# Optimization experiments

Hardware: AMD Instinct MI355X
Metric: run time of the kernel (lower is better)

Reference implementation:

```python
import jax, jax.numpy as jnp
import numpy as np

G, A, HID, NF, L = 512, 32, 256, 11, 4
EMB = HID - 1  # embed_dim = in_node_nf - 1 (condition_time)


def _forward(node_feat, pos, t,
             enc_w1, enc_b1, enc_w2, enc_b2,
             ew1, eb1, ew2, eb2,
             xw1, xb1, xw2, xb2,
             hw1, hb1, hw2, hb2,
             rg1, rgb1, rv1, rvb1, rg2, rgb2, rv2, rvb2, rw3, rb3,
             batch, edge_src, edge_dst):
    silu = jax.nn.silu
    N = node_feat.shape[0]
    # remove_mean_batch: subtract per-graph centroid (scatter_mean)
    cnt = jax.ops.segment_sum(jnp.ones((N, 1), pos.dtype), batch, num_segments=G)
    mean = jax.ops.segment_sum(pos, batch, num_segments=G) / cnt
    x0 = pos - mean[batch]
    # fragment encoder MLP (last layer no activation): 11 -> 22 -> 255
    h = silu(node_feat @ enc_w1 + enc_b1) @ enc_w2 + enc_b2
    # condition on time (t scalar broadcast to all nodes)
    h = jnp.concatenate([h, jnp.full((N, 1), t[0], h.dtype)], axis=1)  # [N, 256]
    x = x0
    for l in range(L):  # EGNN message-passing layers
        hi, hj = h[edge_src], h[edge_dst]
        rel = x[edge_src] - x[edge_dst]                    # [E, 3]
        d2 = jnp.sum(rel * rel, axis=-1, keepdims=True)    # [E, 1]
        e_in = jnp.concatenate([hi, hj, d2], axis=1)       # [E, 2*HID+1]
        m = silu(silu(e_in @ ew1[l] + eb1[l]) @ ew2[l] + eb2[l])  # edge MLP phi_e
        agg = jax.ops.segment_sum(m, edge_src, num_segments=N)
        coef = silu(m @ xw1[l] + xb1[l]) @ xw2[l] + xb2[l]        # phi_x -> [E,1]
        # subgraph_mask is all ones (single fragment), coord update equivariant
        x = x + jax.ops.segment_sum(rel * coef, edge_src, num_segments=N)
        h = h + silu(jnp.concatenate([h, agg], axis=1) @ hw1[l] + hb1[l]) @ hw2[l] + hb2[l]
    # GatedMLP readout: 256 -> 256 -> 256 -> 1, last layer plain linear
    g = silu(h @ rg1 + rgb1) * (h @ rv1 + rvb1)
    g = silu(g @ rg2 + rgb2) * (g @ rv2 + rvb2)
    y = g @ rw3 + rb3                                      # [N, 1]
    ae = jax.ops.segment_sum(y, batch, num_segments=G)[:, 0]  # per-graph energy
    forces = x - x0                                        # equivariant coord displacement
    return ae, forces


def setup_inputs() -> dict:
    key = jax.random.key(0)
    kc = [0]
    def nk():
        kc[0] += 1
        return jax.random.fold_in(key, kc[0])
    N = G * A
    node_feat = jax.random.normal(nk(), (N, NF), jnp.float32)
    pos = jax.random.normal(nk(), (N, 3), jnp.float32) * 3.0
    batch = jnp.repeat(jnp.arange(G), A)
    # fully-connected intra-graph edges without self loops (get_edges_index)
    i = np.arange(A)
    s, d = np.meshgrid(i, i, indexing='ij')
    msk = s != d
    s, d = s[msk], d[msk]
    offs = (np.arange(G) * A)[:, None]
    edge_src = jnp.asarray((s[None, :] + offs).reshape(-1))
    edge_dst = jnp.asarray((d[None, :] + offs).reshape(-1))
    def lin(fi, fo):
        return jax.random.normal(nk(), (fi, fo), jnp.float32) / np.sqrt(fi)
    def linL(fi, fo):
        return jax.random.normal(nk(), (L, fi, fo), jnp.float32) / np.sqrt(fi)
    inp = dict(node_feat=node_feat, pos=pos, t=jnp.zeros((1,), jnp.float32),
               enc_w1=lin(NF, 2 * NF), enc_b1=jnp.zeros((2 * NF,), jnp.float32),
               enc_w2=lin(2 * NF, EMB), enc_b2=jnp.zeros((EMB,), jnp.float32),
               ew1=linL(2 * HID + 1, HID), eb1=jnp.zeros((L, HID), jnp.float32),
               ew2=linL(HID, HID), eb2=jnp.zeros((L, HID), jnp.float32),
               xw1=linL(HID, HID), xb1=jnp.zeros((L, HID), jnp.float32),
               xw2=linL(HID, 1) * 0.1, xb2=jnp.zeros((L, 1), jnp.float32),
               hw1=linL(2 * HID, HID), hb1=jnp.zeros((L, HID), jnp.float32),
               hw2=linL(HID, HID), hb2=jnp.zeros((L, HID), jnp.float32),
               rg1=lin(HID, HID), rgb1=jnp.zeros((HID,), jnp.float32),
               rv1=lin(HID, HID), rvb1=jnp.zeros((HID,), jnp.float32),
               rg2=lin(HID, HID), rgb2=jnp.zeros((HID,), jnp.float32),
               rv2=lin(HID, HID), rvb2=jnp.zeros((HID,), jnp.float32),
               rw3=lin(HID, 1), rb3=jnp.zeros((1,), jnp.float32),
               batch=batch, edge_src=edge_src, edge_dst=edge_dst)
    return inp


def reference(node_feat, pos, t,
              enc_w1, enc_b1, enc_w2, enc_b2,
              ew1, eb1, ew2, eb2,
              xw1, xb1, xw2, xb2,
              hw1, hb1, hw2, hb2,
              rg1, rgb1, rv1, rvb1, rg2, rgb2, rv2, rvb2, rw3, rb3,
              batch, edge_src, edge_dst):
    return _forward(node_feat, pos, t,
                    enc_w1, enc_b1, enc_w2, enc_b2,
                    ew1, eb1, ew2, eb2,
                    xw1, xb1, xw2, xb2,
                    hw1, hb1, hw2, hb2,
                    rg1, rgb1, rv1, rvb1, rg2, rgb2, rv2, rvb2, rw3, rb3,
                    batch, edge_src, edge_dst)
```

## Files before the change

### kernel.cpp

```cpp
#include <hip/hip_runtime.h>

#define NGRAPH 512
#define NA 32
#define HID 256
#define NT 512
#define NLAYER 4

using short8 = __attribute__((ext_vector_type(8))) short;
using f32x4  = __attribute__((ext_vector_type(4))) float;

#define MFMA(a,b,c) __builtin_amdgcn_mfma_f32_16x16x32_bf16((a),(b),(c),0,0,0)

__device__ __forceinline__ float CL(float x) {
    return fminf(fmaxf(x, -1e15f), 1e15f);
}
__device__ __forceinline__ float silu_f(float x) {
    return x / (1.0f + __expf(-x));
}
__device__ __forceinline__ unsigned short bf16t(float x) {
    return (unsigned short)(__float_as_uint(x) >> 16);
}
__device__ __forceinline__ float up16(unsigned short u) {
    return __uint_as_float(((unsigned)u) << 16);
}

__device__ __forceinline__ short8 ldA(const unsigned short* sA, int row, int kk, int sg) {
    return *(const short8*)(sA + row*256 + ((kk*32 + sg*8) ^ ((row & 7) << 3)));
}

__device__ __forceinline__ short8 ldBfrag(const float* __restrict__ W,
                                          int kk, int nt, int li, int sg) {
    const float* p = W + (size_t)(kk*32 + sg*8)*HID + nt*16 + li;
    short8 r;
#pragma unroll
    for (int e = 0; e < 8; ++e) r[e] = (short)bf16t(p[(size_t)e*HID]);
    return r;
}

extern "C" __global__ void __launch_bounds__(NT, 2)
egnn_mfma(const float* __restrict__ node_feat, const float* __restrict__ pos,
          const float* __restrict__ tt,
          const float* __restrict__ enc_w1, const float* __restrict__ enc_b1,
          const float* __restrict__ enc_w2, const float* __restrict__ enc_b2,
          const float* __restrict__ ew1, const float* __restrict__ eb1,
          const float* __restrict__ ew2, const float* __restrict__ eb2,
          const float* __restrict__ xw1, const float* __restrict__ xb1,
          const float* __restrict__ xw2, const float* __restrict__ xb2,
          const float* __restrict__ hw1, const float* __restrict__ hb1,
          const float* __restrict__ hw2, const float* __restrict__ hb2,
          const float* __restrict__ rg1, const float* __restrict__ rgb1,
          const float* __restrict__ rv1, const float* __restrict__ rvb1,
          const float* __restrict__ rg2, const float* __restrict__ rgb2,
          const float* __restrict__ rv2, const float* __restrict__ rvb2,
          const float* __restrict__ rw3, const float* __restrict__ rb3,
          float* __restrict__ out)
{
    __shared__ float          sH  [NA*HID];
    __shared__ unsigned short sPa [NA*HID];
    __shared__ unsigned short sPb [NA*HID];
    __shared__ unsigned short sAgg[NA*HID];
    __shared__ unsigned short sAb [64*HID];
    __shared__ float sW1d[HID];
    __shared__ float sB1 [HID];
    __shared__ float sh_x[NA*3], sh_x0[NA*3], sh_dx[NA*3];
    __shared__ float sh_d2[64], sh_coef[64];
    __shared__ float sh_a1[NA*22];
    __shared__ float sh_red[8];

    const int g    = blockIdx.x;
    const int tid  = threadIdx.x;
    const int w    = tid >> 6;
    const int lane = tid & 63;
    const int li   = lane & 15;
    const int sg   = lane >> 4;
    const int nb   = g * NA;

    if (tid < NA) {
        float px = pos[(nb+tid)*3+0], py = pos[(nb+tid)*3+1], pz = pos[(nb+tid)*3+2];
        float sx = px, sy = py, sz = pz;
#pragma unroll
        for (int m = 1; m < 32; m <<= 1) {
            sx += __shfl_xor(sx, m); sy += __shfl_xor(sy, m); sz += __shfl_xor(sz, m);
        }
        const float inv = 1.0f/32.0f;
        const float xx = px - sx*inv, xy = py - sy*inv, xz = pz - sz*inv;
        sh_x [tid*3+0]=xx; sh_x [tid*3+1]=xy; sh_x [tid*3+2]=xz;
        sh_x0[tid*3+0]=xx; sh_x0[tid*3+1]=xy; sh_x0[tid*3+2]=xz;
        sh_dx[tid*3+0]=0.f; sh_dx[tid*3+1]=0.f; sh_dx[tid*3+2]=0.f;
    }

    for (int e = tid; e < NA*22; e += NT) {
        const int node = e / 22, u = e - node*22;
        const float* nfp = node_feat + (size_t)(nb+node)*11;
        float s = enc_b1[u];
#pragma unroll
        for (int f = 0; f < 11; ++f) s = fmaf(nfp[f], enc_w1[f*22+u], s);
        sh_a1[e] = CL(silu_f(s));
    }
    __syncthreads();
    for (int e = tid; e < NA*255; e += NT) {
        const int node = e / 255, o = e - node*255;
        const float* ap = sh_a1 + node*22;
        float s = enc_b2[o];
#pragma unroll
        for (int u = 0; u < 22; ++u) s = fmaf(ap[u], enc_w2[u*255+o], s);
        sH[node*HID + o] = CL(s);
    }
    if (tid < NA) sH[tid*HID + 255] = tt[0];
    __syncthreads();

    for (int l = 0; l < NLAYER; ++l) {
        const float* W1   = ew1 + (size_t)l*513*HID;
        const float* W1b  = W1 + 256*HID;
        const float* b1v  = eb1 + l*HID;
        const float* W2   = ew2 + (size_t)l*HID*HID;
        const float* b2v  = eb2 + l*HID;
        const float* XW1  = xw1 + (size_t)l*HID*HID;
        const float* xb1v = xb1 + l*HID;
        const float* XW2  = xw2 + (size_t)l*HID;
        const float  xb2v = xb2[l];
        const float* HW1a = hw1 + (size_t)l*2*HID*HID;
        const float* HW1b = HW1a + 256*HID;
        const float* hb1v = hb1 + l*HID;
        const float* HW2  = hw2 + (size_t)l*HID*HID;
        const float* hb2v = hb2 + l*HID;

        for (int t2 = tid; t2 < 1024; t2 += NT) {
            const int row = t2 >> 5, c = t2 & 31;
            const float* hp = sH + row*HID + c*8;
            short8 o;
#pragma unroll
            for (int e = 0; e < 8; ++e) o[e] = (short)bf16t(hp[e]);
            *(short8*)(sAb + row*256 + ((c*8) ^ ((row & 7) << 3))) = o;
        }
        if (tid < HID) { sW1d[tid] = W1[512*HID + tid]; sB1[tid] = b1v[tid]; }
        __syncthreads();

        {
            const int mg = w >> 2, ng = w & 3;
            f32x4 aA[4] = {}, aB[4] = {};
#pragma unroll
            for (int kk = 0; kk < 8; ++kk) {
                short8 a = ldA(sAb, mg*16 + li, kk, sg);
#pragma unroll
                for (int q = 0; q < 4; ++q) {
                    aA[q] = MFMA(a, ldBfrag(W1,  kk, ng*4+q, li, sg), aA[q]);
                    aB[q] = MFMA(a, ldBfrag(W1b, kk, ng*4+q, li, sg), aB[q]);
                }
            }
#pragma unroll
            for (int q = 0; q < 4; ++q) {
                const int col = (ng*4+q)*16 + li;
#pragma unroll
                for (int r = 0; r < 4; ++r) {
                    const int row = mg*16 + sg*4 + r;
                    sPa[row*256 + col] = bf16t(CL(aA[q][r]));
                    sPb[row*256 + col] = bf16t(CL(aB[q][r]));
                }
            }
        }
        short8 w2f[16], x1f[16];
#pragma unroll
        for (int kk = 0; kk < 8; ++kk)
#pragma unroll
            for (int q = 0; q < 2; ++q) {
                w2f[kk*2+q] = ldBfrag(W2,  kk, w*2+q, li, sg);
                x1f[kk*2+q] = ldBfrag(XW1, kk, w*2+q, li, sg);
            }
        __syncthreads();

        for (int pair = 0; pair < 16; ++pair) {
            const int i0 = pair*2;
            if (tid < 64) {
                const int ip = tid >> 5, j = tid & 31, ig = i0 + ip;
                const float rx = sh_x[ig*3+0]-sh_x[j*3+0];
                const float ry = sh_x[ig*3+1]-sh_x[j*3+1];
                const float rz = sh_x[ig*3+2]-sh_x[j*3+2];
                sh_d2[tid] = rx*rx + ry*ry + rz*rz;
                sh_coef[tid] = 0.f;
            }
            __syncthreads();

            {
                const int c = tid & 31, rg = tid >> 5;
                const float4* wp = (const float4*)(sW1d + c*8);
                const float4* bp = (const float4*)(sB1 + c*8);
                const float4 w0 = wp[0], w1 = wp[1], b0 = bp[0], b1 = bp[1];
                float wd[8] = {w0.x,w0.y,w0.z,w0.w,w1.x,w1.y,w1.z,w1.w};
                float bb[8] = {b0.x,b0.y,b0.z,b0.w,b1.x,b1.y,b1.z,b1.w};
#pragma unroll
                for (int k = 0; k < 4; ++k) {
                    const int row = rg + 16*k;
                    const int ip = row >> 5, j = row & 31;
                    const short8 pa8 = *(const short8*)(sPa + (i0+ip)*256 + c*8);
                    const short8 pb8 = *(const short8*)(sPb + j*256 + c*8);
                    const float d2v = sh_d2[row];
                    short8 o;
#pragma unroll
                    for (int e = 0; e < 8; ++e) {
                        float x = up16((unsigned short)pa8[e]) + up16((unsigned short)pb8[e])
                                + d2v*wd[e] + bb[e];
                        o[e] = (short)bf16t(CL(silu_f(x)));
                    }
                    *(short8*)(sAb + row*256 + ((c*8) ^ ((row & 7) << 3))) = o;
                }
            }
            __syncthreads();

            f32x4 a1[4][2] = {};
#pragma unroll
            for (int kk = 0; kk < 8; ++kk)
#pragma unroll
                for (int mt = 0; mt < 4; ++mt) {
                    short8 a = ldA(sAb, mt*16 + li, kk, sg);
                    a1[mt][0] = MFMA(a, w2f[kk*2+0], a1[mt][0]);
                    a1[mt][1] = MFMA(a, w2f[kk*2+1], a1[mt][1]);
                }
#pragma unroll
            for (int q = 0; q < 2; ++q) {
                const float b2c = b2v[(w*2+q)*16 + li];
#pragma unroll
                for (int mt = 0; mt < 4; ++mt)
#pragma unroll
                    for (int r = 0; r < 4; ++r)
                        a1[mt][q][r] = CL(silu_f(a1[mt][q][r] + b2c));
            }
#pragma unroll
            for (int ip = 0; ip < 2; ++ip) {
                const int ig = i0 + ip;
                const int drow = ip*32 + ig;
#pragma unroll
                for (int q = 0; q < 2; ++q) {
                    float s = 0.f;
#pragma unroll
                    for (int mt2 = 0; mt2 < 2; ++mt2) {
                        const int mt = ip*2 + mt2;
#pragma unroll
                        for (int r = 0; r < 4; ++r) {
                            const int row = mt*16 + sg*4 + r;
                            s += (row == drow) ? 0.f : a1[mt][q][r];
                        }
                    }
                    s += __shfl_xor(s, 16);
                    s += __shfl_xor(s, 32);
                    if (lane < 16) {
                        const int col = (w*2+q)*16 + lane;
                        sAgg[ig*256 + (col ^ ((ig & 7) << 3))] = bf16t(CL(s));
                    }
                }
            }
            __syncthreads();

#pragma unroll
            for (int q = 0; q < 2; ++q) {
                const int col = (w*2+q)*16 + li;
#pragma unroll
                for (int mt = 0; mt < 4; ++mt)
#pragma unroll
                    for (int r = 0; r < 4; ++r) {
                        const int row = mt*16 + sg*4 + r;
                        sAb[row*256 + (col ^ ((row & 7) << 3))] = bf16t(a1[mt][q][r]);
                    }
            }
            __syncthreads();

            f32x4 a2[4][2] = {};
#pragma unroll
            for (int kk = 0; kk < 8; ++kk)
#pragma unroll
                for (int mt = 0; mt < 4; ++mt) {
                    short8 a = ldA(sAb, mt*16 + li, kk, sg);
                    a2[mt][0] = MFMA(a, x1f[kk*2+0], a2[mt][0]);
                    a2[mt][1] = MFMA(a, x1f[kk*2+1], a2[mt][1]);
                }
            {
                const float xbc0 = xb1v[(w*2+0)*16 + li], xwc0 = XW2[(w*2+0)*16 + li];
                const float xbc1 = xb1v[(w*2+1)*16 + li], xwc1 = XW2[(w*2+1)*16 + li];
#pragma unroll
                for (int mt = 0; mt < 4; ++mt) {
                    float p[4];
#pragma unroll
                    for (int r = 0; r < 4; ++r)
                        p[r] = silu_f(a2[mt][0][r] + xbc0) * xwc0
                             + silu_f(a2[mt][1][r] + xbc1) * xwc1;
#pragma unroll
                    for (int r = 0; r < 4; ++r) {
                        float v = p[r];
                        v += __shfl_xor(v, 1); v += __shfl_xor(v, 2);
                        v += __shfl_xor(v, 4); v += __shfl_xor(v, 8);
                        if (li == 0) atomicAdd(&sh_coef[mt*16 + sg*4 + r], CL(v));
                    }
                }
            }
            __syncthreads();

            if (tid < 64) {
                const int ip = tid >> 5, j = tid & 31, ig = i0 + ip;
                const float cf = CL(sh_coef[tid] + xb2v);
                const float rx = sh_x[ig*3+0]-sh_x[j*3+0];
                const float ry = sh_x[ig*3+1]-sh_x[j*3+1];
                const float rz = sh_x[ig*3+2]-sh_x[j*3+2];
                const bool diag = (j == ig);
                float vx = diag ? 0.f : rx*cf;
                float vy = diag ? 0.f : ry*cf;
                float vz = diag ? 0.f : rz*cf;
#pragma unroll
                for (int m = 1; m < 32; m <<= 1) {
                    vx += __shfl_xor(vx, m); vy += __shfl_xor(vy, m); vz += __shfl_xor(vz, m);
                }
                if ((tid & 31) == 0) {
                    sh_dx[ig*3+0] = CL(sh_dx[ig*3+0] + vx);
                    sh_dx[ig*3+1] = CL(sh_dx[ig*3+1] + vy);
                    sh_dx[ig*3+2] = CL(sh_dx[ig*3+2] + vz);
                }
            }
            __syncthreads();
        }

        for (int t2 = tid; t2 < 1024; t2 += NT) {
            const int row = t2 >> 5, c = t2 & 31;
            const float* hp = sH + row*HID + c*8;
            short8 o;
#pragma unroll
            for (int e = 0; e < 8; ++e) o[e] = (short)bf16t(hp[e]);
            *(short8*)(sAb + row*256 + ((c*8) ^ ((row & 7) << 3))) = o;
        }
        if (tid < NA*3) { sh_x[tid] = CL(sh_x[tid] + sh_dx[tid]); sh_dx[tid] = 0.f; }
        __syncthreads();

        {
            const int mg = w >> 2, ng = w & 3;
            f32x4 u[4] = {};
#pragma unroll
            for (int kk = 0; kk < 8; ++kk) {
                short8 ah = ldA(sAb,  mg*16 + li, kk, sg);
                short8 ag = ldA(sAgg, mg*16 + li, kk, sg);
#pragma unroll
                for (int q = 0; q < 4; ++q) {
                    u[q] = MFMA(ah, ldBfrag(HW1a, kk, ng*4+q, li, sg), u[q]);
                    u[q] = MFMA(ag, ldBfrag(HW1b, kk, ng*4+q, li, sg), u[q]);
                }
            }
#pragma unroll
            for (int q = 0; q < 4; ++q) {
                const int col = (ng*4+q)*16 + li;
                const float bc = hb1v[col];
#pragma unroll
                for (int r = 0; r < 4; ++r) {
                    const int row32 = 32 + mg*16 + sg*4 + r;
                    sAb[row32*256 + (col ^ ((row32 & 7) << 3))] =
                        bf16t(CL(silu_f(u[q][r] + bc)));
                }
            }
            __syncthreads();
            f32x4 d[4] = {};
#pragma unroll
            for (int kk = 0; kk < 8; ++kk) {
                short8 a = ldA(sAb, 32 + mg*16 + li, kk, sg);
#pragma unroll
                for (int q = 0; q < 4; ++q)
                    d[q] = MFMA(a, ldBfrag(HW2, kk, ng*4+q, li, sg), d[q]);
            }
#pragma unroll
            for (int q = 0; q < 4; ++q) {
                const int col = (ng*4+q)*16 + li;
                const float bc = hb2v[col];
#pragma unroll
                for (int r = 0; r < 4; ++r) {
                    const int idx = (mg*16 + sg*4 + r)*HID + col;
                    sH[idx] = CL(sH[idx] + d[q][r] + bc);
                }
            }
        }
        __syncthreads();
    }

    for (int t2 = tid; t2 < 1024; t2 += NT) {
        const int row = t2 >> 5, c = t2 & 31;
        const float* hp = sH + row*HID + c*8;
        short8 o;
#pragma unroll
        for (int e = 0; e < 8; ++e) o[e] = (short)bf16t(hp[e]);
        *(short8*)(sAb + row*256 + ((c*8) ^ ((row & 7) << 3))) = o;
    }
    __syncthreads();
    {
        const int mg = w >> 2, ng = w & 3;
        f32x4 ga[4] = {}, gb[4] = {};
#pragma unroll
        for (int kk = 0; kk < 8; ++kk) {
            short8 a = ldA(sAb, mg*16 + li, kk, sg);
#pragma unroll
            for (int q = 0; q < 4; ++q) {
                ga[q] = MFMA(a, ldBfrag(rg1, kk, ng*4+q, li, sg), ga[q]);
                gb[q] = MFMA(a, ldBfrag(rv1, kk, ng*4+q, li, sg), gb[q]);
            }
        }
#pragma unroll
        for (int q = 0; q < 4; ++q) {
            const int col = (ng*4+q)*16 + li;
            const float bg = rgb1[col], bv = rvb1[col];
#pragma unroll
            for (int r = 0; r < 4; ++r) {
                const int row32 = 32 + mg*16 + sg*4 + r;
                sAb[row32*256 + (col ^ ((row32 & 7) << 3))] =
                    bf16t(CL(silu_f(ga[q][r] + bg) * (gb[q][r] + bv)));
            }
        }
        __syncthreads();
        f32x4 g2a[4] = {}, g2b[4] = {};
#pragma unroll
        for (int kk = 0; kk < 8; ++kk) {
            short8 a = ldA(sAb, 32 + mg*16 + li, kk, sg);
#pragma unroll
            for (int q = 0; q < 4; ++q) {
                g2a[q] = MFMA(a, ldBfrag(rg2, kk, ng*4+q, li, sg), g2a[q]);
                g2b[q] = MFMA(a, ldBfrag(rv2, kk, ng*4+q, li, sg), g2b[q]);
            }
        }
        float p = 0.f;
#pragma unroll
        for (int q = 0; q < 4; ++q) {
            const int col = (ng*4+q)*16 + li;
            const float bg = rgb2[col], bv = rvb2[col], rw = rw3[col];
#pragma unroll
            for (int r = 0; r < 4; ++r)
                p += CL(silu_f(g2a[q][r] + bg) * (g2b[q][r] + bv)) * rw;
        }
        p = CL(p);
#pragma unroll
        for (int m = 1; m < 64; m <<= 1) p += __shfl_xor(p, m);
        if (lane == 0) sh_red[w] = p;
        __syncthreads();
        if (tid == 0) {
            float s = 0.f;
#pragma unroll
            for (int ww = 0; ww < 8; ++ww) s += sh_red[ww];
            out[g] = s + (float)NA * rb3[0];
        }
    }
    if (tid < NA*3) out[NGRAPH + g*(NA*3) + tid] = sh_x[tid] - sh_x0[tid];
}

extern "C" __global__ void egnn_node_pad1() {}
extern "C" __global__ void egnn_node_pad2() {}

extern "C" void kernel_launch(void* const* d_in, const int* in_sizes, int n_in,
                              void* d_out, int out_size, void* d_ws, size_t ws_size,
                              hipStream_t stream)
{
    const float* node_feat = (const float*)d_in[0];
    const float* pos    = (const float*)d_in[1];
    const float* tt     = (const float*)d_in[2];
    const float* enc_w1 = (const float*)d_in[3];
    const float* enc_b1 = (const float*)d_in[4];
    const float* enc_w2 = (const float*)d_in[5];
    const float* enc_b2 = (const float*)d_in[6];
    const float* ew1    = (const float*)d_in[7];
    const float* eb1    = (const float*)d_in[8];
    const float* ew2    = (const float*)d_in[9];
    const float* eb2    = (const float*)d_in[10];
    const float* xw1    = (const float*)d_in[11];
    const float* xb1    = (const float*)d_in[12];
    const float* xw2    = (const float*)d_in[13];
    const float* xb2    = (const float*)d_in[14];
    const float* hw1    = (const float*)d_in[15];
    const float* hb1    = (const float*)d_in[16];
    const float* hw2    = (const float*)d_in[17];
    const float* hb2    = (const float*)d_in[18];
    const float* rg1    = (const float*)d_in[19];
    const float* rgb1   = (const float*)d_in[20];
    const float* rv1    = (const float*)d_in[21];
    const float* rvb1   = (const float*)d_in[22];
    const float* rg2    = (const float*)d_in[23];
    const float* rgb2   = (const float*)d_in[24];
    const float* rv2    = (const float*)d_in[25];
    const float* rvb2   = (const float*)d_in[26];
    const float* rw3    = (const float*)d_in[27];
    const float* rb3    = (const float*)d_in[28];
    (void)d_ws; (void)ws_size; (void)in_sizes; (void)n_in;

    egnn_mfma<<<NGRAPH, NT, 0, stream>>>(
        node_feat, pos, tt, enc_w1, enc_b1, enc_w2, enc_b2,
        ew1, eb1, ew2, eb2, xw1, xb1, xw2, xb2,
        hw1, hb1, hw2, hb2, rg1, rgb1, rv1, rvb1,
        rg2, rgb2, rv2, rvb2, rw3, rb3,
        (float*)d_out);
    egnn_node_pad1<<<1, 64, 0, stream>>>();
    egnn_node_pad2<<<1, 64, 0, stream>>>();
}
```

Measured before the change: 2.454 ms.

## Store node features as bf16, split GEMMs by weight half, precompute pairwise distances

Node hidden state is now kept in shared memory as swizzled bf16 instead of fp32, which removes the per-layer fp32-to-bf16 conversion passes. The node-level GEMMs are redistributed so each wave group handles one weight half (or gate/value matrix) over all 32 rows. Each B fragment is therefore loaded once and reused across two row tiles, and partial sums are combined through an fp32 scratch buffer aliased onto sAb. Pairwise squared distances are computed once per layer, and the coefficient buffer is double-buffered, which drops one barrier per pair iteration. Rounding the residual stream to bf16 adds precision loss, and the extra reduction barriers plus the shared-memory layout changes could affect occupancy.

```diff
diff --git a/kernel.cpp b/kernel.cpp
--- a/kernel.cpp
+++ b/kernel.cpp
@@ -23,11 +23,12 @@
 __device__ __forceinline__ float up16(unsigned short u) {
     return __uint_as_float(((unsigned)u) << 16);
 }
-
+__device__ __forceinline__ int swzi(int row, int col) {
+    return row*256 + (col ^ ((row & 7) << 3));
+}
 __device__ __forceinline__ short8 ldA(const unsigned short* sA, int row, int kk, int sg) {
     return *(const short8*)(sA + row*256 + ((kk*32 + sg*8) ^ ((row & 7) << 3)));
 }
-
 __device__ __forceinline__ short8 ldBfrag(const float* __restrict__ W,
                                           int kk, int nt, int li, int sg) {
     const float* p = W + (size_t)(kk*32 + sg*8)*HID + nt*16 + li;
@@ -37,7 +38,8 @@
     return r;
 }
 
-extern "C" __global__ void __launch_bounds__(NT, 2)
+extern "C" __global__ void __launch_bounds__(NT)
+__attribute__((amdgpu_waves_per_eu(2, 2)))
 egnn_mfma(const float* __restrict__ node_feat, const float* __restrict__ pos,
           const float* __restrict__ tt,
           const float* __restrict__ enc_w1, const float* __restrict__ enc_b1,
@@ -55,17 +57,19 @@
           const float* __restrict__ rw3, const float* __restrict__ rb3,
           float* __restrict__ out)
 {
-    __shared__ float          sH  [NA*HID];
+    __shared__ unsigned short sHb [NA*HID];
     __shared__ unsigned short sPa [NA*HID];
     __shared__ unsigned short sPb [NA*HID];
     __shared__ unsigned short sAgg[NA*HID];
-    __shared__ unsigned short sAb [64*HID];
-    __shared__ float sW1d[HID];
-    __shared__ float sB1 [HID];
+    __shared__ unsigned short sAb [2*NA*HID];
+    __shared__ float sD2[NA*NA];
+    __shared__ float sW1d[HID], sB1[HID];
     __shared__ float sh_x[NA*3], sh_x0[NA*3], sh_dx[NA*3];
-    __shared__ float sh_d2[64], sh_coef[64];
+    __shared__ float sh_coef[2][64];
     __shared__ float sh_a1[NA*22];
     __shared__ float sh_red[8];
+
+    float* sF = (float*)sAb;
 
     const int g    = blockIdx.x;
     const int tid  = threadIdx.x;
@@ -79,8 +83,8 @@
         float px = pos[(nb+tid)*3+0], py = pos[(nb+tid)*3+1], pz = pos[(nb+tid)*3+2];
         float sx = px, sy = py, sz = pz;
 #pragma unroll
-        for (int m = 1; m < 32; m <<= 1) {
-            sx += __shfl_xor(sx, m); sy += __shfl_xor(sy, m); sz += __shfl_xor(sz, m);
+        for (int mm = 1; mm < 32; mm <<= 1) {
+            sx += __shfl_xor(sx, mm); sy += __shfl_xor(sy, mm); sz += __shfl_xor(sz, mm);
         }
         const float inv = 1.0f/32.0f;
         const float xx = px - sx*inv, xy = py - sy*inv, xz = pz - sz*inv;
@@ -104,14 +108,13 @@
         float s = enc_b2[o];
 #pragma unroll
         for (int u = 0; u < 22; ++u) s = fmaf(ap[u], enc_w2[u*255+o], s);
-        sH[node*HID + o] = CL(s);
+        sHb[swzi(node, o)] = bf16t(CL(s));
     }
-    if (tid < NA) sH[tid*HID + 255] = tt[0];
+    if (tid < NA) sHb[swzi(tid, 255)] = bf16t(tt[0]);
     __syncthreads();
 
     for (int l = 0; l < NLAYER; ++l) {
         const float* W1   = ew1 + (size_t)l*513*HID;
-        const float* W1b  = W1 + 256*HID;
         const float* b1v  = eb1 + l*HID;
         const float* W2   = ew2 + (size_t)l*HID*HID;
         const float* b2v  = eb2 + l*HID;
@@ -119,45 +122,46 @@
         const float* xb1v = xb1 + l*HID;
         const float* XW2  = xw2 + (size_t)l*HID;
         const float  xb2v = xb2[l];
-        const float* HW1a = hw1 + (size_t)l*2*HID*HID;
-        const float* HW1b = HW1a + 256*HID;
+        const float* HW1  = hw1 + (size_t)l*2*HID*HID;
         const float* hb1v = hb1 + l*HID;
         const float* HW2  = hw2 + (size_t)l*HID*HID;
         const float* hb2v = hb2 + l*HID;
 
-        for (int t2 = tid; t2 < 1024; t2 += NT) {
-            const int row = t2 >> 5, c = t2 & 31;
-            const float* hp = sH + row*HID + c*8;
-            short8 o;
-#pragma unroll
-            for (int e = 0; e < 8; ++e) o[e] = (short)bf16t(hp[e]);
-            *(short8*)(sAb + row*256 + ((c*8) ^ ((row & 7) << 3))) = o;
+        for (int e = tid; e < NA*NA; e += NT) {
+            const int i = e >> 5, j = e & 31;
+            const float rx = sh_x[i*3+0]-sh_x[j*3+0];
+            const float ry = sh_x[i*3+1]-sh_x[j*3+1];
+            const float rz = sh_x[i*3+2]-sh_x[j*3+2];
+            sD2[e] = rx*rx + ry*ry + rz*rz;
         }
         if (tid < HID) { sW1d[tid] = W1[512*HID + tid]; sB1[tid] = b1v[tid]; }
-        __syncthreads();
 
         {
-            const int mg = w >> 2, ng = w & 3;
-            f32x4 aA[4] = {}, aB[4] = {};
+            const int m = w >> 2, s = w & 3;
+            const float* Wm = W1 + (size_t)m*256*HID;
+            f32x4 acc[2][4] = {};
 #pragma unroll
             for (int kk = 0; kk < 8; ++kk) {
-                short8 a = ldA(sAb, mg*16 + li, kk, sg);
+                const short8 a0 = ldA(sHb, li,      kk, sg);
+                const short8 a1_= ldA(sHb, 16 + li, kk, sg);
 #pragma unroll
                 for (int q = 0; q < 4; ++q) {
-                    aA[q] = MFMA(a, ldBfrag(W1,  kk, ng*4+q, li, sg), aA[q]);
-                    aB[q] = MFMA(a, ldBfrag(W1b, kk, ng*4+q, li, sg), aB[q]);
-                }
-            }
-#pragma unroll
-            for (int q = 0; q < 4; ++q) {
-                const int col = (ng*4+q)*16 + li;
-#pragma unroll
-                for (int r = 0; r < 4; ++r) {
-                    const int row = mg*16 + sg*4 + r;
-                    sPa[row*256 + col] = bf16t(CL(aA[q][r]));
-                    sPb[row*256 + col] = bf16t(CL(aB[q][r]));
-                }
-            }
+                    const short8 b = ldBfrag(Wm, kk, s*4+q, li, sg);
+                    acc[0][q] = MFMA(a0,  b, acc[0][q]);
+                    acc[1][q] = MFMA(a1_, b, acc[1][q]);
+                }
+            }
+            unsigned short* dst = m ? sPb : sPa;
+#pragma unroll
+            for (int mt = 0; mt < 2; ++mt)
+#pragma unroll
+                for (int q = 0; q < 4; ++q)
+#pragma unroll
+                    for (int r = 0; r < 4; ++r) {
+                        const int row = mt*16 + sg*4 + r;
+                        const int col = (s*4+q)*16 + li;
+                        dst[swzi(row, col)] = bf16t(CL(acc[mt][q][r]));
+                    }
         }
         short8 w2f[16], x1f[16];
 #pragma unroll
@@ -167,42 +171,43 @@
                 w2f[kk*2+q] = ldBfrag(W2,  kk, w*2+q, li, sg);
                 x1f[kk*2+q] = ldBfrag(XW1, kk, w*2+q, li, sg);
             }
+        const float b2c[2] = { b2v[(w*2+0)*16+li],  b2v[(w*2+1)*16+li]  };
+        const float xbc[2] = { xb1v[(w*2+0)*16+li], xb1v[(w*2+1)*16+li] };
+        const float xwc[2] = { XW2[(w*2+0)*16+li],  XW2[(w*2+1)*16+li]  };
         __syncthreads();
 
-        for (int pair = 0; pair < 16; ++pair) {
+        int par = 0;
+        for (int pair = 0; pair < 16; ++pair, par ^= 1) {
             const int i0 = pair*2;
-            if (tid < 64) {
-                const int ip = tid >> 5, j = tid & 31, ig = i0 + ip;
-                const float rx = sh_x[ig*3+0]-sh_x[j*3+0];
-                const float ry = sh_x[ig*3+1]-sh_x[j*3+1];
-                const float rz = sh_x[ig*3+2]-sh_x[j*3+2];
-                sh_d2[tid] = rx*rx + ry*ry + rz*rz;
-                sh_coef[tid] = 0.f;
-            }
-            __syncthreads();
-
+            if (tid < 64) sh_coef[par][tid] = 0.f;
             {
                 const int c = tid & 31, rg = tid >> 5;
                 const float4* wp = (const float4*)(sW1d + c*8);
                 const float4* bp = (const float4*)(sB1 + c*8);
-                const float4 w0 = wp[0], w1 = wp[1], b0 = bp[0], b1 = bp[1];
-                float wd[8] = {w0.x,w0.y,w0.z,w0.w,w1.x,w1.y,w1.z,w1.w};
-                float bb[8] = {b0.x,b0.y,b0.z,b0.w,b1.x,b1.y,b1.z,b1.w};
+                const float4 w0 = wp[0], w1 = wp[1], bq0 = bp[0], bq1 = bp[1];
+                const float wd[8] = {w0.x,w0.y,w0.z,w0.w,w1.x,w1.y,w1.z,w1.w};
+                const float bb[8] = {bq0.x,bq0.y,bq0.z,bq0.w,bq1.x,bq1.y,bq1.z,bq1.w};
+                const short8 paA = *(const short8*)(sPa + (i0+0)*256 + ((c*8) ^ (((i0+0)&7)<<3)));
+                const short8 paB = *(const short8*)(sPa + (i0+1)*256 + ((c*8) ^ (((i0+1)&7)<<3)));
+                float pab0[8], pab1[8];
+#pragma unroll
+                for (int e = 0; e < 8; ++e) {
+                    pab0[e] = up16((unsigned short)paA[e]) + bb[e];
+                    pab1[e] = up16((unsigned short)paB[e]) + bb[e];
+                }
 #pragma unroll
                 for (int k = 0; k < 4; ++k) {
                     const int row = rg + 16*k;
-                    const int ip = row >> 5, j = row & 31;
-                    const short8 pa8 = *(const short8*)(sPa + (i0+ip)*256 + c*8);
-                    const short8 pb8 = *(const short8*)(sPb + j*256 + c*8);
-                    const float d2v = sh_d2[row];
+                    const int j   = rg + 16*(k & 1);
+                    const float d2v = sD2[(i0 + (k>>1))*32 + j];
+                    const short8 pb8 = *(const short8*)(sPb + j*256 + ((c*8) ^ ((j&7)<<3)));
                     short8 o;
 #pragma unroll
                     for (int e = 0; e < 8; ++e) {
-                        float x = up16((unsigned short)pa8[e]) + up16((unsigned short)pb8[e])
-                                + d2v*wd[e] + bb[e];
-                        o[e] = (short)bf16t(CL(silu_f(x)));
+                        const float base = (k>>1) ? pab1[e] : pab0[e];
+                        o[e] = (short)bf16t(CL(silu_f(base + up16((unsigned short)pb8[e]) + d2v*wd[e])));
                     }
-                    *(short8*)(sAb + row*256 + ((c*8) ^ ((row & 7) << 3))) = o;
+                    *(short8*)(sAb + row*256 + ((c*8) ^ ((row&7)<<3))) = o;
                 }
             }
             __syncthreads();
@@ -212,19 +217,17 @@
             for (int kk = 0; kk < 8; ++kk)
 #pragma unroll
                 for (int mt = 0; mt < 4; ++mt) {
-                    short8 a = ldA(sAb, mt*16 + li, kk, sg);
+                    const short8 a = ldA(sAb, mt*16 + li, kk, sg);
                     a1[mt][0] = MFMA(a, w2f[kk*2+0], a1[mt][0]);
                     a1[mt][1] = MFMA(a, w2f[kk*2+1], a1[mt][1]);
                 }
 #pragma unroll
-            for (int q = 0; q < 2; ++q) {
-                const float b2c = b2v[(w*2+q)*16 + li];
+            for (int q = 0; q < 2; ++q)
 #pragma unroll
                 for (int mt = 0; mt < 4; ++mt)
 #pragma unroll
                     for (int r = 0; r < 4; ++r)
-                        a1[mt][q][r] = CL(silu_f(a1[mt][q][r] + b2c));
-            }
+                        a1[mt][q][r] = CL(silu_f(a1[mt][q][r] + b2c[q]));
 #pragma unroll
             for (int ip = 0; ip < 2; ++ip) {
                 const int ig = i0 + ip;
@@ -243,25 +246,19 @@
                     }
                     s += __shfl_xor(s, 16);
                     s += __shfl_xor(s, 32);
-                    if (lane < 16) {
-                        const int col = (w*2+q)*16 + lane;
-                        sAgg[ig*256 + (col ^ ((ig & 7) << 3))] = bf16t(CL(s));
-                    }
-                }
-            }
-            __syncthreads();
-
-#pragma unroll
-            for (int q = 0; q < 2; ++q) {
-                const int col = (w*2+q)*16 + li;
+                    if (lane < 16)
+                        sAgg[swzi(ig, (w*2+q)*16 + lane)] = bf16t(CL(s));
+                }
+            }
+            __syncthreads();
+
+#pragma unroll
+            for (int q = 0; q < 2; ++q)
 #pragma unroll
                 for (int mt = 0; mt < 4; ++mt)
 #pragma unroll
-                    for (int r = 0; r < 4; ++r) {
-                        const int row = mt*16 + sg*4 + r;
-                        sAb[row*256 + (col ^ ((row & 7) << 3))] = bf16t(a1[mt][q][r]);
-                    }
-            }
+                    for (int r = 0; r < 4; ++r)
+                        sAb[swzi(mt*16 + sg*4 + r, (w*2+q)*16 + li)] = bf16t(a1[mt][q][r]);
             __syncthreads();
 
             f32x4 a2[4][2] = {};
@@ -269,34 +266,26 @@
             for (int kk = 0; kk < 8; ++kk)
 #pragma unroll
                 for (int mt = 0; mt < 4; ++mt) {
-                    short8 a = ldA(sAb, mt*16 + li, kk, sg);
+                    const short8 a = ldA(sAb, mt*16 + li, kk, sg);
                     a2[mt][0] = MFMA(a, x1f[kk*2+0], a2[mt][0]);
                     a2[mt][1] = MFMA(a, x1f[kk*2+1], a2[mt][1]);
                 }
-            {
-                const float xbc0 = xb1v[(w*2+0)*16 + li], xwc0 = XW2[(w*2+0)*16 + li];
-                const float xbc1 = xb1v[(w*2+1)*16 + li], xwc1 = XW2[(w*2+1)*16 + li];
-#pragma unroll
-                for (int mt = 0; mt < 4; ++mt) {
-                    float p[4];
-#pragma unroll
-                    for (int r = 0; r < 4; ++r)
-                        p[r] = silu_f(a2[mt][0][r] + xbc0) * xwc0
-                             + silu_f(a2[mt][1][r] + xbc1) * xwc1;
-#pragma unroll
-                    for (int r = 0; r < 4; ++r) {
-                        float v = p[r];
-                        v += __shfl_xor(v, 1); v += __shfl_xor(v, 2);
-                        v += __shfl_xor(v, 4); v += __shfl_xor(v, 8);
-                        if (li == 0) atomicAdd(&sh_coef[mt*16 + sg*4 + r], CL(v));
-                    }
+#pragma unroll
+            for (int mt = 0; mt < 4; ++mt) {
+#pragma unroll
+                for (int r = 0; r < 4; ++r) {
+                    float v = silu_f(a2[mt][0][r] + xbc[0]) * xwc[0]
+                            + silu_f(a2[mt][1][r] + xbc[1]) * xwc[1];
+                    v += __shfl_xor(v, 1); v += __shfl_xor(v, 2);
+                    v += __shfl_xor(v, 4); v += __shfl_xor(v, 8);
+                    if (li == 0) atomicAdd(&sh_coef[par][mt*16 + sg*4 + r], CL(v));
                 }
             }
             __syncthreads();
 
             if (tid < 64) {
                 const int ip = tid >> 5, j = tid & 31, ig = i0 + ip;
-                const float cf = CL(sh_coef[tid] + xb2v);
+                const float cf = CL(sh_coef[par][tid] + xb2v);
                 const float rx = sh_x[ig*3+0]-sh_x[j*3+0];
                 const float ry = sh_x[ig*3+1]-sh_x[j*3+1];
                 const float rz = sh_x[ig*3+2]-sh_x[j*3+2];
@@ -305,8 +294,8 @@
                 float vy = diag ? 0.f : ry*cf;
                 float vz = diag ? 0.f : rz*cf;
 #pragma unroll
-                for (int m = 1; m < 32; m <<= 1) {
-                    vx += __shfl_xor(vx, m); vy += __shfl_xor(vy, m); vz += __shfl_xor(vz, m);
+                for (int mm = 1; mm < 32; mm <<= 1) {
+                    vx += __shfl_xor(vx, mm); vy += __shfl_xor(vy, mm); vz += __shfl_xor(vz, mm);
                 }
                 if ((tid & 31) == 0) {
                     sh_dx[ig*3+0] = CL(sh_dx[ig*3+0] + vx);
@@ -314,128 +303,179 @@
                     sh_dx[ig*3+2] = CL(sh_dx[ig*3+2] + vz);
                 }
             }
-            __syncthreads();
-        }
-
-        for (int t2 = tid; t2 < 1024; t2 += NT) {
-            const int row = t2 >> 5, c = t2 & 31;
-            const float* hp = sH + row*HID + c*8;
-            short8 o;
-#pragma unroll
-            for (int e = 0; e < 8; ++e) o[e] = (short)bf16t(hp[e]);
-            *(short8*)(sAb + row*256 + ((c*8) ^ ((row & 7) << 3))) = o;
-        }
+        }
+        __syncthreads();
+
         if (tid < NA*3) { sh_x[tid] = CL(sh_x[tid] + sh_dx[tid]); sh_dx[tid] = 0.f; }
+
+        {
+            const int kh = w >> 2, s = w & 3;
+            const unsigned short* Amat = kh ? sAgg : sHb;
+            const float* Bmat = HW1 + (size_t)kh*256*HID;
+            f32x4 acc[2][4] = {};
+#pragma unroll
+            for (int kk = 0; kk < 8; ++kk) {
+                const short8 a0 = ldA(Amat, li,      kk, sg);
+                const short8 a1_= ldA(Amat, 16 + li, kk, sg);
+#pragma unroll
+                for (int q = 0; q < 4; ++q) {
+                    const short8 b = ldBfrag(Bmat, kk, s*4+q, li, sg);
+                    acc[0][q] = MFMA(a0,  b, acc[0][q]);
+                    acc[1][q] = MFMA(a1_, b, acc[1][q]);
+                }
+            }
+            if (kh == 0) {
+#pragma unroll
+                for (int mt = 0; mt < 2; ++mt)
+#pragma unroll
+                    for (int q = 0; q < 4; ++q)
+#pragma unroll
+                        for (int r = 0; r < 4; ++r)
+                            sF[(mt*16+sg*4+r)*256 + (s*4+q)*16 + li] = acc[mt][q][r];
+            }
+            __syncthreads();
+            if (kh == 1) {
+#pragma unroll
+                for (int mt = 0; mt < 2; ++mt)
+#pragma unroll
+                    for (int q = 0; q < 4; ++q)
+#pragma unroll
+                        for (int r = 0; r < 4; ++r) {
+                            const int row = mt*16+sg*4+r, col = (s*4+q)*16+li;
+                            const float u = CL(silu_f(sF[row*256+col] + acc[mt][q][r] + hb1v[col]));
+                            sPa[swzi(row, col)] = bf16t(u);
+                        }
+            }
+        }
         __syncthreads();
-
         {
-            const int mg = w >> 2, ng = w & 3;
-            f32x4 u[4] = {};
-#pragma unroll
-            for (int kk = 0; kk < 8; ++kk) {
-                short8 ah = ldA(sAb,  mg*16 + li, kk, sg);
-                short8 ag = ldA(sAgg, mg*16 + li, kk, sg);
+            const int kh = w >> 2, s = w & 3;
+            f32x4 acc[2][4] = {};
+#pragma unroll
+            for (int kk4 = 0; kk4 < 4; ++kk4) {
+                const int kk = kh*4 + kk4;
+                const short8 a0 = ldA(sPa, li,      kk, sg);
+                const short8 a1_= ldA(sPa, 16 + li, kk, sg);
 #pragma unroll
                 for (int q = 0; q < 4; ++q) {
-                    u[q] = MFMA(ah, ldBfrag(HW1a, kk, ng*4+q, li, sg), u[q]);
-                    u[q] = MFMA(ag, ldBfrag(HW1b, kk, ng*4+q, li, sg), u[q]);
-                }
-            }
-#pragma unroll
-            for (int q = 0; q < 4; ++q) {
-                const int col = (ng*4+q)*16 + li;
-                const float bc = hb1v[col];
-#pragma unroll
-                for (int r = 0; r < 4; ++r) {
-                    const int row32 = 32 + mg*16 + sg*4 + r;
-                    sAb[row32*256 + (col ^ ((row32 & 7) << 3))] =
-                        bf16t(CL(silu_f(u[q][r] + bc)));
-                }
-            }
-            __syncthreads();
-            f32x4 d[4] = {};
-#pragma unroll
-            for (int kk = 0; kk < 8; ++kk) {
-                short8 a = ldA(sAb, 32 + mg*16 + li, kk, sg);
-#pragma unroll
-                for (int q = 0; q < 4; ++q)
-                    d[q] = MFMA(a, ldBfrag(HW2, kk, ng*4+q, li, sg), d[q]);
-            }
-#pragma unroll
-            for (int q = 0; q < 4; ++q) {
-                const int col = (ng*4+q)*16 + li;
-                const float bc = hb2v[col];
-#pragma unroll
-                for (int r = 0; r < 4; ++r) {
-                    const int idx = (mg*16 + sg*4 + r)*HID + col;
-                    sH[idx] = CL(sH[idx] + d[q][r] + bc);
-                }
+                    const short8 b = ldBfrag(HW2, kk, s*4+q, li, sg);
+                    acc[0][q] = MFMA(a0,  b, acc[0][q]);
+                    acc[1][q] = MFMA(a1_, b, acc[1][q]);
+                }
+            }
+            if (kh == 0) {
+#pragma unroll
+                for (int mt = 0; mt < 2; ++mt)
+#pragma unroll
+                    for (int q = 0; q < 4; ++q)
+#pragma unroll
+                        for (int r = 0; r < 4; ++r)
+                            sF[(mt*16+sg*4+r)*256 + (s*4+q)*16 + li] = acc[mt][q][r];
+            }
+            __syncthreads();
+            if (kh == 1) {
+#pragma unroll
+                for (int mt = 0; mt < 2; ++mt)
+#pragma unroll
+                    for (int q = 0; q < 4; ++q)
+#pragma unroll
+                        for (int r = 0; r < 4; ++r) {
+                            const int row = mt*16+sg*4+r, col = (s*4+q)*16+li;
+                            const int idx = swzi(row, col);
+                            sHb[idx] = bf16t(CL(up16(sHb[idx]) + sF[row*256+col]
+                                                + acc[mt][q][r] + hb2v[col]));
+                        }
             }
         }
         __syncthreads();
     }
 
-    for (int t2 = tid; t2 < 1024; t2 += NT) {
-        const int row = t2 >> 5, c = t2 & 31;
-        const float* hp = sH + row*HID + c*8;
-        short8 o;
-#pragma unroll
-        for (int e = 0; e < 8; ++e) o[e] = (short)bf16t(hp[e]);
-        *(short8*)(sAb + row*256 + ((c*8) ^ ((row & 7) << 3))) = o;
-    }
-    __syncthreads();
     {
-        const int mg = w >> 2, ng = w & 3;
-        f32x4 ga[4] = {}, gb[4] = {};
-#pragma unroll
-        for (int kk = 0; kk < 8; ++kk) {
-            short8 a = ldA(sAb, mg*16 + li, kk, sg);
-#pragma unroll
-            for (int q = 0; q < 4; ++q) {
-                ga[q] = MFMA(a, ldBfrag(rg1, kk, ng*4+q, li, sg), ga[q]);
-                gb[q] = MFMA(a, ldBfrag(rv1, kk, ng*4+q, li, sg), gb[q]);
-            }
-        }
-#pragma unroll
-        for (int q = 0; q < 4; ++q) {
-            const int col = (ng*4+q)*16 + li;
-            const float bg = rgb1[col], bv = rvb1[col];
-#pragma unroll
-            for (int r = 0; r < 4; ++r) {
-                const int row32 = 32 + mg*16 + sg*4 + r;
-                sAb[row32*256 + (col ^ ((row32 & 7) << 3))] =
-                    bf16t(CL(silu_f(ga[q][r] + bg) * (gb[q][r] + bv)));
+        const int mrole = w >> 2, s = w & 3;
+        {
+            const float* G = mrole ? rv1 : rg1;
+            f32x4 acc[2][4] = {};
+#pragma unroll
+            for (int kk = 0; kk < 8; ++kk) {
+                const short8 a0 = ldA(sHb, li,      kk, sg);
+                const short8 a1_= ldA(sHb, 16 + li, kk, sg);
+#pragma unroll
+                for (int q = 0; q < 4; ++q) {
+                    const short8 b = ldBfrag(G, kk, s*4+q, li, sg);
+                    acc[0][q] = MFMA(a0,  b, acc[0][q]);
+                    acc[1][q] = MFMA(a1_, b, acc[1][q]);
+                }
+            }
+            if (mrole == 0) {
+#pragma unroll
+                for (int mt = 0; mt < 2; ++mt)
+#pragma unroll
+                    for (int q = 0; q < 4; ++q)
+#pragma unroll
+                        for (int r = 0; r < 4; ++r)
+                            sF[(mt*16+sg*4+r)*256 + (s*4+q)*16 + li] = acc[mt][q][r];
+            }
+            __syncthreads();
+            if (mrole == 1) {
+#pragma unroll
+                for (int mt = 0; mt < 2; ++mt)
+#pragma unroll
+                    for (int q = 0; q < 4; ++q)
+#pragma unroll
+                        for (int r = 0; r < 4; ++r) {
+                            const int row = mt*16+sg*4+r, col = (s*4+q)*16+li;
+                            const float v = CL(silu_f(sF[row*256+col] + rgb1[col])
+                                               * (acc[mt][q][r] + rvb1[col]));
+                            sPb[swzi(row, col)] = bf16t(v);
+                        }
             }
         }
         __syncthreads();
-        f32x4 g2a[4] = {}, g2b[4] = {};
-#pragma unroll
-        for (int kk = 0; kk < 8; ++kk) {
-            short8 a = ldA(sAb, 32 + mg*16 + li, kk, sg);
-#pragma unroll
-            for (int q = 0; q < 4; ++q) {
-                g2a[q] = MFMA(a, ldBfrag(rg2, kk, ng*4+q, li, sg), g2a[q]);
-                g2b[q] = MFMA(a, ldBfrag(rv2, kk, ng*4+q, li, sg), g2b[q]);
-            }
-        }
-        float p = 0.f;
-#pragma unroll
-        for (int q = 0; q < 4; ++q) {
-            const int col = (ng*4+q)*16 + li;
-            const float bg = rgb2[col], bv = rvb2[col], rw = rw3[col];
-#pragma unroll
-            for (int r = 0; r < 4; ++r)
-                p += CL(silu_f(g2a[q][r] + bg) * (g2b[q][r] + bv)) * rw;
-        }
-        p = CL(p);
-#pragma unroll
-        for (int m = 1; m < 64; m <<= 1) p += __shfl_xor(p, m);
-        if (lane == 0) sh_red[w] = p;
+        {
+            const float* G = mrole ? rv2 : rg2;
+            f32x4 acc[2][4] = {};
+#pragma unroll
+            for (int kk = 0; kk < 8; ++kk) {
+                const short8 a0 = ldA(sPb, li,      kk, sg);
+                const short8 a1_= ldA(sPb, 16 + li, kk, sg);
+#pragma unroll
+                for (int q = 0; q < 4; ++q) {
+                    const short8 b = ldBfrag(G, kk, s*4+q, li, sg);
+                    acc[0][q] = MFMA(a0,  b, acc[0][q]);
+                    acc[1][q] = MFMA(a1_, b, acc[1][q]);
+                }
+            }
+            if (mrole == 0) {
+#pragma unroll
+                for (int mt = 0; mt < 2; ++mt)
+#pragma unroll
+                    for (int q = 0; q < 4; ++q)
+#pragma unroll
+                        for (int r = 0; r < 4; ++r)
+                            sF[(mt*16+sg*4+r)*256 + (s*4+q)*16 + li] = acc[mt][q][r];
+            }
+            __syncthreads();
+            if (mrole == 1) {
+                float p = 0.f;
+#pragma unroll
+                for (int mt = 0; mt < 2; ++mt)
+#pragma unroll
+                    for (int q = 0; q < 4; ++q)
+#pragma unroll
+                        for (int r = 0; r < 4; ++r) {
+                            const int row = mt*16+sg*4+r, col = (s*4+q)*16+li;
+                            p += CL(silu_f(sF[row*256+col] + rgb2[col])
+                                    * (acc[mt][q][r] + rvb2[col])) * rw3[col];
+                        }
+                p = CL(p);
+#pragma unroll
+                for (int mm = 1; mm < 64; mm <<= 1) p += __shfl_xor(p, mm);
+                if (lane == 0) sh_red[w] = p;
+            }
+        }
         __syncthreads();
         if (tid == 0) {
-            float s = 0.f;
-#pragma unroll
-            for (int ww = 0; ww < 8; ++ww) s += sh_red[ww];
+            float s = sh_red[4] + sh_red[5] + sh_red[6] + sh_red[7];
             out[g] = s + (float)NA * rb3[0];
         }
     }
```

Measured after the change: 2.157 ms. -12.1%, faster.
